# Kernel tuning notes

Measured on AMD Instinct MI355X. Metric: run time of the kernel, lower is better.

The kernel has to match this reference:

```python
import jax, jax.numpy as jnp
import numpy as np

D_MODEL = 1024
NUM_HEADS = 16
D_K = D_MODEL // NUM_HEADS
D_FF = 4096
EPS = 1e-5


def setup_inputs() -> dict:
    key = jax.random.key(0)
    ks = jax.random.split(key, 16)
    B, S = 2, 2048
    s_attn = 1.0 / np.sqrt(D_MODEL)
    s_ff1 = 1.0 / np.sqrt(D_MODEL)
    s_ff2 = 1.0 / np.sqrt(D_FF)
    return {
        "x": jax.random.normal(ks[0], (B, S, D_MODEL), jnp.float32),
        "Wq": jax.random.normal(ks[1], (D_MODEL, D_MODEL), jnp.float32) * s_attn,
        "bq": jnp.zeros((D_MODEL,), jnp.float32),
        "Wk": jax.random.normal(ks[2], (D_MODEL, D_MODEL), jnp.float32) * s_attn,
        "bk": jnp.zeros((D_MODEL,), jnp.float32),
        "Wv": jax.random.normal(ks[3], (D_MODEL, D_MODEL), jnp.float32) * s_attn,
        "bv": jnp.zeros((D_MODEL,), jnp.float32),
        "Wo": jax.random.normal(ks[4], (D_MODEL, D_MODEL), jnp.float32) * s_attn,
        "bo": jnp.zeros((D_MODEL,), jnp.float32),
        "W1": jax.random.normal(ks[5], (D_MODEL, D_FF), jnp.float32) * s_ff1,
        "b1": jnp.zeros((D_FF,), jnp.float32),
        "W2": jax.random.normal(ks[6], (D_FF, D_MODEL), jnp.float32) * s_ff2,
        "b2": jnp.zeros((D_MODEL,), jnp.float32),
        "g1": jnp.ones((D_MODEL,), jnp.float32),
        "be1": jnp.zeros((D_MODEL,), jnp.float32),
        "g2": jnp.ones((D_MODEL,), jnp.float32),
        "be2": jnp.zeros((D_MODEL,), jnp.float32),
    }


def _layernorm(x, g, b):
    m = jnp.mean(x, axis=-1, keepdims=True)
    v = jnp.mean(jnp.square(x - m), axis=-1, keepdims=True)
    return (x - m) * jax.lax.rsqrt(v + EPS) * g + b


def _split_heads(x, B, S):
    # (B, S, D) -> (B, H, S, d_k)
    return x.reshape(B, S, NUM_HEADS, D_K).transpose(0, 2, 1, 3)


def reference(x, Wq, bq, Wk, bk, Wv, bv, Wo, bo, W1, b1, W2, b2, g1, be1, g2, be2):
    B, S, _ = x.shape
    Q = _split_heads(x @ Wq + bq, B, S)
    K = _split_heads(x @ Wk + bk, B, S)
    V = _split_heads(x @ Wv + bv, B, S)
    scores = jnp.einsum("bhqd,bhkd->bhqk", Q, K) / np.sqrt(D_K).astype(np.float32)
    attn = jax.nn.softmax(scores, axis=-1)  # dropout is identity (p=0 / eval)
    ctx = jnp.einsum("bhqk,bhkd->bhqd", attn, V)
    ctx = ctx.transpose(0, 2, 1, 3).reshape(B, S, D_MODEL)
    attn_out = ctx @ Wo + bo
    h = _layernorm(x + attn_out, g1, be1)
    ff = jax.nn.relu(h @ W1 + b1) @ W2 + b2
    out = _layernorm(h + ff, g2, be2)
    return out, attn
```

## Files before the change

### kernel.cpp

```cpp
#include <hip/hip_runtime.h>
#include <cstddef>
#include <cstdint>

#define D_MODEL 1024
#define NUM_HEADS 16
#define DK 64
#define D_FF 4096
#define SEQ 2048
#define BATCH 2
#define EPS 1e-5f

typedef unsigned short u16;
typedef __attribute__((ext_vector_type(8))) short bf16x8;
typedef __attribute__((ext_vector_type(8))) unsigned short us8;
typedef __attribute__((ext_vector_type(4))) unsigned short us4;
typedef __attribute__((ext_vector_type(4))) float f32x4;

#define SBAR() asm volatile("s_barrier" ::: "memory")

__device__ __forceinline__ u16 f2b(float f) {
    unsigned u = __float_as_uint(f);
    u += 0x7fffu + ((u >> 16) & 1u);
    return (u16)(u >> 16);
}
__device__ __forceinline__ float b2f(u16 v) {
    return __uint_as_float((unsigned)v << 16);
}

__device__ __forceinline__ void gload16(const void* g, void* l) {
    __builtin_amdgcn_global_load_lds(
        (const __attribute__((address_space(1))) void*)g,
        (__attribute__((address_space(3))) void*)l, 16, 0, 0);
}

__device__ __forceinline__ void stage_half(
    const u16* __restrict__ g, int ld, long kbase, int h,
    u16* dst, int tid, int wid)
{
#pragma unroll
    for (int r = 0; r < 2; ++r) {
        const int ci  = r * 512 + tid;
        const int row = ci >> 2;
        const int wd  = ci & 3;
        const int f   = (row + (row >> 2)) & 3;
        const long src = (long)row * ld + kbase + (long)(h * 4 + (wd ^ f)) * 8;
        gload16(g + src, dst + (r * 512 + wid * 64) * 8);
    }
}

__device__ __forceinline__ bf16x8 frag64(const u16* base, int ks, int row, int g) {
    const int f = (row + (row >> 2)) & 3;
    return *(const bf16x8*)&base[ks * 8192 + row * 32 + ((g ^ f) * 8)];
}

template<int KTOT, bool RELU>
__global__ __launch_bounds__(512, 2) void gemm256(
    const u16* __restrict__ Abf, const u16* __restrict__ BT,
    const float* __restrict__ bias0, u16* __restrict__ C0,
    int ldc, int nx)
{
    constexpr int NT = KTOT / 64;
    __shared__ u16 lds[2][32768];

    const int tid = threadIdx.x;
    const int wid = tid >> 6, l = tid & 63;
    const int r16 = l & 15, g = l >> 4;
    const int wr = wid >> 2, wc = wid & 3;

    const int nwg = gridDim.x;
    const int q = nwg >> 3, rr = nwg & 7;
    const int xcd = blockIdx.x & 7, idx = blockIdx.x >> 3;
    const int wg = (xcd < rr ? xcd * (q + 1) : rr * (q + 1) + (xcd - rr) * q) + idx;
    const long bm = (long)(wg / nx) * 256;
    const long bn = (long)(wg % nx) * 256;

    const u16* Ag = Abf + bm * KTOT;
    const u16* Bg = BT + bn * KTOT;

    f32x4 acc[8][4];
#pragma unroll
    for (int i = 0; i < 8; ++i)
#pragma unroll
        for (int n = 0; n < 4; ++n)
            acc[i][n] = (f32x4){0.f, 0.f, 0.f, 0.f};

    stage_half(Ag, KTOT, 0, 0, &lds[0][0],     tid, wid);
    stage_half(Ag, KTOT, 0, 1, &lds[0][8192],  tid, wid);
    stage_half(Bg, KTOT, 0, 0, &lds[0][16384], tid, wid);
    stage_half(Bg, KTOT, 0, 1, &lds[0][24576], tid, wid);
    if (NT > 1) {
        stage_half(Ag, KTOT, 64, 0, &lds[1][0],     tid, wid);
        stage_half(Bg, KTOT, 64, 0, &lds[1][16384], tid, wid);
    }
    asm volatile("s_waitcnt vmcnt(4)" ::: "memory");
    SBAR();

    for (int t = 0; t < NT; ++t) {
        u16* cur = &lds[t & 1][0];
        u16* nxt = &lds[(t + 1) & 1][0];
        const long k1 = (long)(t + 1) * 64;
        const long k2 = (long)(t + 2) * 64;
        const bool s1 = (t + 1 < NT), s2 = (t + 2 < NT);

        bf16x8 a0[4], b0[4];
#pragma unroll
        for (int i = 0; i < 4; ++i) {
            a0[i] = frag64(cur,         0, wr * 128 + i * 16 + r16, g);
            b0[i] = frag64(cur + 16384, 0, wc * 64  + i * 16 + r16, g);
        }
        if (s1) stage_half(Ag, KTOT, k1, 1, nxt + 8192, tid, wid);
        SBAR();
        __builtin_amdgcn_s_setprio(1);
#pragma unroll
        for (int i = 0; i < 4; ++i)
#pragma unroll
            for (int n = 0; n < 4; ++n)
                acc[i][n] = __builtin_amdgcn_mfma_f32_16x16x32_bf16(
                    a0[i], b0[n], acc[i][n], 0, 0, 0);
        __builtin_amdgcn_s_setprio(0);
        SBAR();

        bf16x8 a1[4];
#pragma unroll
        for (int i = 0; i < 4; ++i)
            a1[i] = frag64(cur, 0, wr * 128 + (i + 4) * 16 + r16, g);
        if (s1) stage_half(Bg, KTOT, k1, 1, nxt + 24576, tid, wid);
        SBAR();
        __builtin_amdgcn_s_setprio(1);
#pragma unroll
        for (int i = 0; i < 4; ++i)
#pragma unroll
            for (int n = 0; n < 4; ++n)
                acc[i + 4][n] = __builtin_amdgcn_mfma_f32_16x16x32_bf16(
                    a1[i], b0[n], acc[i + 4][n], 0, 0, 0);
        __builtin_amdgcn_s_setprio(0);
        SBAR();

        bf16x8 a2[4], b1[4];
#pragma unroll
        for (int i = 0; i < 4; ++i) {
            a2[i] = frag64(cur,         1, wr * 128 + i * 16 + r16, g);
            b1[i] = frag64(cur + 16384, 1, wc * 64  + i * 16 + r16, g);
        }
        if (s2) stage_half(Ag, KTOT, k2, 0, cur, tid, wid);
        SBAR();
        __builtin_amdgcn_s_setprio(1);
#pragma unroll
        for (int i = 0; i < 4; ++i)
#pragma unroll
            for (int n = 0; n < 4; ++n)
                acc[i][n] = __builtin_amdgcn_mfma_f32_16x16x32_bf16(
                    a2[i], b1[n], acc[i][n], 0, 0, 0);
        __builtin_amdgcn_s_setprio(0);
        SBAR();

        bf16x8 a3[4];
#pragma unroll
        for (int i = 0; i < 4; ++i)
            a3[i] = frag64(cur, 1, wr * 128 + (i + 4) * 16 + r16, g);
        if (s2) stage_half(Bg, KTOT, k2, 0, cur + 16384, tid, wid);
        SBAR();
        __builtin_amdgcn_s_setprio(1);
#pragma unroll
        for (int i = 0; i < 4; ++i)
#pragma unroll
            for (int n = 0; n < 4; ++n)
                acc[i + 4][n] = __builtin_amdgcn_mfma_f32_16x16x32_bf16(
                    a3[i], b1[n], acc[i + 4][n], 0, 0, 0);
        __builtin_amdgcn_s_setprio(0);
        if (s2)      asm volatile("s_waitcnt vmcnt(4)" ::: "memory");
        else if (s1) asm volatile("s_waitcnt vmcnt(0)" ::: "memory");
        SBAR();
    }

    const long crow0 = bm + wr * 128 + g * 4;
    const long ccol0 = bn + wc * 64 + r16;
#pragma unroll
    for (int n = 0; n < 4; ++n) {
        const long col = ccol0 + n * 16;
        const float bv = bias0[col];
#pragma unroll
        for (int i = 0; i < 8; ++i)
#pragma unroll
            for (int j = 0; j < 4; ++j) {
                const long row = crow0 + i * 16 + j;
                float v = acc[i][n][j] + bv;
                if (RELU) v = fmaxf(v, 0.f);
                C0[row * (long)ldc + col] = f2b(v);
            }
    }
}

template<bool RELU, int NSPLIT>
__global__ __launch_bounds__(256) void gemm_mfma(
    const u16* __restrict__ Abf, const u16* __restrict__ BT,
    const float* __restrict__ bias0, const float* __restrict__ bias1,
    const float* __restrict__ bias2,
    u16* __restrict__ C0, u16* __restrict__ C1, u16* __restrict__ C2,
    int lda, int ldb, int ldc, int K, int nx)
{
    constexpr int BM = 128, BN = 128;
    constexpr int MI = 4, NI = 4;
    constexpr int RA = 2, RB = 2;
    constexpr int TILE = (BM + BN) * 32;

    __shared__ u16 sm[3][TILE];

    const int tid = threadIdx.x;
    const int w = tid >> 6, l = tid & 63;
    const int r16 = l & 15, g = l >> 4;
    const int wr = w >> 1, wc = w & 1;

    const int nwg = gridDim.x;
    const int q = nwg >> 3, rr = nwg & 7;
    const int xcd = blockIdx.x & 7, idx = blockIdx.x >> 3;
    const int wg = (xcd < rr ? xcd * (q + 1) : rr * (q + 1) + (xcd - rr) * q) + idx;
    const long bm = (long)(wg / nx) * BM;
    const long bn = (long)(wg % nx) * BN;

    f32x4 acc[MI][NI];
#pragma unroll
    for (int mi = 0; mi < MI; ++mi)
#pragma unroll
        for (int ni = 0; ni < NI; ++ni)
            acc[mi][ni] = (f32x4){0.f, 0.f, 0.f, 0.f};

    long aOff[RA], bOff[RB];
#pragma unroll
    for (int r = 0; r < RA; ++r) {
        int c = r * 256 + tid;
        aOff[r] = (long)(bm + (c >> 2)) * lda + (c & 3) * 8;
    }
#pragma unroll
    for (int r = 0; r < RB; ++r) {
        int c = r * 256 + tid;
        bOff[r] = (long)(bn + (c >> 2)) * ldb + (c & 3) * 8;
    }

#pragma unroll
    for (int r = 0; r < RA; ++r)
        gload16(Abf + aOff[r], &sm[0][0] + (r * 256 + w * 64) * 8);
#pragma unroll
    for (int r = 0; r < RB; ++r)
        gload16(BT + bOff[r], &sm[0][BM * 32] + (r * 256 + w * 64) * 8);
    if (K > 32) {
#pragma unroll
        for (int r = 0; r < RA; ++r)
            gload16(Abf + aOff[r] + 32, &sm[1][0] + (r * 256 + w * 64) * 8);
#pragma unroll
        for (int r = 0; r < RB; ++r)
            gload16(BT + bOff[r] + 32, &sm[1][BM * 32] + (r * 256 + w * 64) * 8);
    }
    asm volatile("s_waitcnt vmcnt(4)" ::: "memory");
    SBAR();

    int cur = 0;
    for (int k0 = 0; k0 < K; k0 += 32) {
        const int nx2 = (cur >= 1) ? cur - 1 : cur + 2;
        if (k0 + 64 < K) {
#pragma unroll
            for (int r = 0; r < RA; ++r)
                gload16(Abf + aOff[r] + k0 + 64, &sm[nx2][0] + (r * 256 + w * 64) * 8);
#pragma unroll
            for (int r = 0; r < RB; ++r)
                gload16(BT + bOff[r] + k0 + 64, &sm[nx2][BM * 32] + (r * 256 + w * 64) * 8);
        }

        const u16* smA = &sm[cur][0];
        const u16* smB = &sm[cur][BM * 32];
        bf16x8 af[MI], bfr[NI];
#pragma unroll
        for (int mi = 0; mi < MI; ++mi)
            af[mi] = *(const bf16x8*)&smA[(wr * 64 + mi * 16 + r16) * 32 + g * 8];
#pragma unroll
        for (int ni = 0; ni < NI; ++ni)
            bfr[ni] = *(const bf16x8*)&smB[(wc * 64 + ni * 16 + r16) * 32 + g * 8];
#pragma unroll
        for (int mi = 0; mi < MI; ++mi)
#pragma unroll
            for (int ni = 0; ni < NI; ++ni)
                acc[mi][ni] = __builtin_amdgcn_mfma_f32_16x16x32_bf16(
                    af[mi], bfr[ni], acc[mi][ni], 0, 0, 0);

        if (k0 + 64 < K)      asm volatile("s_waitcnt vmcnt(4)" ::: "memory");
        else if (k0 + 32 < K) asm volatile("s_waitcnt vmcnt(0)" ::: "memory");
        SBAR();
        cur = (cur == 2) ? 0 : cur + 1;
    }

    u16* Cb = C0; const float* bp = bias0; long coff = 0;
    if (NSPLIT == 3) {
        const int grp = (int)(bn >> 10);
        if (grp == 1)      { Cb = C1; bp = bias1; }
        else if (grp == 2) { Cb = C2; bp = bias2; }
        coff = (long)grp << 10;
    }
    const long crow0 = bm + wr * 64 + g * 4;
    const long ccol0 = bn + wc * 64 + r16 - coff;
#pragma unroll
    for (int ni = 0; ni < NI; ++ni) {
        const long col = ccol0 + ni * 16;
        const float bv = bp[col];
#pragma unroll
        for (int mi = 0; mi < MI; ++mi) {
#pragma unroll
            for (int j = 0; j < 4; ++j) {
                const long row = crow0 + mi * 16 + j;
                float v = acc[mi][ni][j] + bv;
                if (RELU) v = fmaxf(v, 0.f);
                Cb[row * (long)ldc + col] = f2b(v);
            }
        }
    }
}

template<bool RELU>
__global__ __launch_bounds__(256) void gemm_n64(
    const u16* __restrict__ Abf, const u16* __restrict__ BT,
    const float* __restrict__ bias, u16* __restrict__ C,
    int lda, int ldb, int ldc, int K, int nx)
{
    constexpr int TILE = 12288;
    __shared__ u16 sm[3][TILE];

    const int tid = threadIdx.x;
    const int w = tid >> 6, l = tid & 63;
    const int r16 = l & 15, g = l >> 4;

    const int nwg = gridDim.x;
    const int q = nwg >> 3, rr = nwg & 7;
    const int xcd = blockIdx.x & 7, idx = blockIdx.x >> 3;
    const int wg = (xcd < rr ? xcd * (q + 1) : rr * (q + 1) + (xcd - rr) * q) + idx;
    const long bm = (long)(wg / nx) * 128;
    const long bn = (long)(wg % nx) * 64;

    f32x4 acc[2][4];
#pragma unroll
    for (int mi = 0; mi < 2; ++mi)
#pragma unroll
        for (int ni = 0; ni < 4; ++ni)
            acc[mi][ni] = (f32x4){0.f, 0.f, 0.f, 0.f};

    long aOff[4], bOff[2];
#pragma unroll
    for (int r = 0; r < 4; ++r) {
        int c = r * 256 + tid;
        int row = c >> 3, sl = c & 7;
        aOff[r] = (long)(bm + row) * lda + (long)(sl ^ (row & 7)) * 8;
    }
#pragma unroll
    for (int r = 0; r < 2; ++r) {
        int c = r * 256 + tid;
        int row = c >> 3, sl = c & 7;
        bOff[r] = (long)(bn + row) * ldb + (long)(sl ^ (row & 7)) * 8;
    }

#define N64_STAGE(buf, koff)                                                  \
    {                                                                         \
        _Pragma("unroll")                                                     \
        for (int r = 0; r < 4; ++r)                                           \
            gload16(Abf + aOff[r] + (koff), &sm[buf][0] + (r * 256 + w * 64) * 8); \
        _Pragma("unroll")                                                     \
        for (int r = 0; r < 2; ++r)                                           \
            gload16(BT + bOff[r] + (koff), &sm[buf][8192] + (r * 256 + w * 64) * 8); \
    }

    N64_STAGE(0, 0)
    if (K > 64) N64_STAGE(1, 64)
    asm volatile("s_waitcnt vmcnt(6)" ::: "memory");
    SBAR();

    int cur = 0;
    for (int k0 = 0; k0 < K; k0 += 64) {
        const int nx2 = (cur >= 1) ? cur - 1 : cur + 2;
        if (k0 + 128 < K) N64_STAGE(nx2, k0 + 128)

        const u16* smA = &sm[cur][0];
        const u16* smB = &sm[cur][8192];
#pragma unroll
        for (int ks = 0; ks < 2; ++ks) {
            bf16x8 af[2], bfr[4];
#pragma unroll
            for (int mi = 0; mi < 2; ++mi)
                af[mi] = *(const bf16x8*)
                    &smA[(w * 32 + mi * 16 + r16) * 64 + (((ks * 4 + g) ^ (r16 & 7)) * 8)];
#pragma unroll
            for (int ni = 0; ni < 4; ++ni)
                bfr[ni] = *(const bf16x8*)
                    &smB[(ni * 16 + r16) * 64 + (((ks * 4 + g) ^ (r16 & 7)) * 8)];
            __builtin_amdgcn_s_setprio(1);
#pragma unroll
            for (int mi = 0; mi < 2; ++mi)
#pragma unroll
                for (int ni = 0; ni < 4; ++ni)
                    acc[mi][ni] = __builtin_amdgcn_mfma_f32_16x16x32_bf16(
                        af[mi], bfr[ni], acc[mi][ni], 0, 0, 0);
            __builtin_amdgcn_s_setprio(0);
        }

        if (k0 + 128 < K)      asm volatile("s_waitcnt vmcnt(6)" ::: "memory");
        else if (k0 + 64 < K)  asm volatile("s_waitcnt vmcnt(0)" ::: "memory");
        SBAR();
        cur = (cur == 2) ? 0 : cur + 1;
    }
#undef N64_STAGE

    const long crow0 = bm + w * 32 + g * 4;
    const long ccol0 = bn + r16;
#pragma unroll
    for (int ni = 0; ni < 4; ++ni) {
        const long col = ccol0 + ni * 16;
        const float bv = bias[col];
#pragma unroll
        for (int mi = 0; mi < 2; ++mi) {
#pragma unroll
            for (int j = 0; j < 4; ++j) {
                const long row = crow0 + mi * 16 + j;
                float v = acc[mi][ni][j] + bv;
                if (RELU) v = fmaxf(v, 0.f);
                C[row * (long)ldc + col] = f2b(v);
            }
        }
    }
}

#define QBLK 128
#define KB2 128
#define NT2 (SEQ / KB2)
#define C2E 0.18033688f

__global__ __launch_bounds__(256) void flash_attn(
    const u16* __restrict__ Qg, const u16* __restrict__ Kg,
    const u16* __restrict__ Vt, float* __restrict__ attn,
    u16* __restrict__ ctx)
{
    __shared__ u16 smem[32768];
    __shared__ u16 Ps[4][2048];

    const int tid = threadIdx.x;
    const int w = tid >> 6, l = tid & 63;
    const int r16 = l & 15, g = l >> 4;

    const int wg = (blockIdx.x & 7) * (gridDim.x >> 3) + (blockIdx.x >> 3);
    const int qb = wg & 15, z = wg >> 4;
    const int b = z >> 4, h = z & 15;
    const long q0 = (long)qb * QBLK;

    const long kBase = ((long)b * SEQ) * D_MODEL + h * DK;
    const long vBase = (long)z * DK * SEQ;

    u16* const Qs = smem + 24576;

#pragma unroll
    for (int r = 0; r < 4; ++r) {
        int c = r * 256 + tid;
        int row = c >> 3, bl = c & 7;
        gload16(Qg + ((long)b * SEQ + q0 + row) * D_MODEL + h * DK + ((bl ^ (row & 7)) * 8),
                Qs + (r * 256 + w * 64) * 8);
    }
#define STAGE_K(dst, kro)                                                     \
    {                                                                         \
        _Pragma("unroll")                                                     \
        for (int r = 0; r < 4; ++r) {                                         \
            int c = r * 256 + tid;                                            \
            int row = c >> 3, bl = c & 7;                                     \
            gload16(Kg + kBase + ((kro) + row) * (long)D_MODEL + ((bl ^ (row & 7)) * 8), \
                    (dst) + (r * 256 + w * 64) * 8);                          \
        }                                                                     \
    }
#define STAGE_V(dst, kro)                                                     \
    {                                                                         \
        _Pragma("unroll")                                                     \
        for (int r = 0; r < 4; ++r) {                                         \
            int c = r * 256 + tid;                                            \
            int row = c >> 4, bl = c & 15;                                    \
            gload16(Vt + vBase + (long)row * SEQ + (kro) + ((bl ^ (row & 15)) * 8), \
                    (dst) + (r * 256 + w * 64) * 8);                          \
        }                                                                     \
    }

    STAGE_K(smem, 0)
    STAGE_K(smem + 16384, KB2)
    __syncthreads();

    bf16x8 qf[2][2];
#pragma unroll
    for (int qi = 0; qi < 2; ++qi)
#pragma unroll
        for (int ks = 0; ks < 2; ++ks)
            qf[qi][ks] = *(const bf16x8*)
                &Qs[(w * 32 + qi * 16 + r16) * 64 + (((ks * 4 + g) ^ (r16 & 7)) * 8)];
    __syncthreads();

    float lrun[2] = {0.f, 0.f};

    for (int t = 0; t < NT2; ++t) {
        const int m3n = (t + 2) % 3;
        u16* kdst = (m3n == 0) ? smem : (m3n == 1) ? smem + 16384 : smem + 8192;
        if (t + 2 < NT2) STAGE_K(kdst, (long)(t + 2) * KB2)
        const int m3c = t % 3;
        const u16* kcur = (m3c == 0) ? smem : (m3c == 1) ? smem + 16384 : smem + 8192;

#pragma unroll
        for (int sub = 0; sub < 2; ++sub) {
            f32x4 sT[4][2];
#pragma unroll
            for (int ki = 0; ki < 4; ++ki)
#pragma unroll
                for (int qi = 0; qi < 2; ++qi) sT[ki][qi] = (f32x4){0.f, 0.f, 0.f, 0.f};

            __builtin_amdgcn_s_setprio(1);
#pragma unroll
            for (int ks = 0; ks < 2; ++ks) {
                bf16x8 kf[4];
#pragma unroll
                for (int ki = 0; ki < 4; ++ki)
                    kf[ki] = *(const bf16x8*)
                        &kcur[(sub * 64 + ki * 16 + r16) * 64 + (((ks * 4 + g) ^ (r16 & 7)) * 8)];
#pragma unroll
                for (int ki = 0; ki < 4; ++ki)
#pragma unroll
                    for (int qi = 0; qi < 2; ++qi)
                        sT[ki][qi] = __builtin_amdgcn_mfma_f32_16x16x32_bf16(
                            kf[ki], qf[qi][ks], sT[ki][qi], 0, 0, 0);
            }
            __builtin_amdgcn_s_setprio(0);

#pragma unroll
            for (int qi = 0; qi < 2; ++qi) {
                float ls = 0.f;
#pragma unroll
                for (int ki = 0; ki < 4; ++ki)
#pragma unroll
                    for (int j = 0; j < 4; ++j)
                        ls += exp2f(sT[ki][qi][j] * C2E);
                ls += __shfl_xor(ls, 16);
                ls += __shfl_xor(ls, 32);
                lrun[qi] += ls;
            }
        }
        if (t + 2 < NT2)      asm volatile("s_waitcnt vmcnt(4)" ::: "memory");
        else if (t + 1 < NT2) asm volatile("s_waitcnt vmcnt(0)" ::: "memory");
        if (t + 1 < NT2) SBAR();
    }

    const float il[2] = {1.0f / lrun[0], 1.0f / lrun[1]};

    __syncthreads();
    STAGE_K(smem, 0)
    STAGE_V(smem + 8192, 0)
    __syncthreads();

    f32x4 acc2[2][4];
#pragma unroll
    for (int mi = 0; mi < 2; ++mi)
#pragma unroll
        for (int ni = 0; ni < 4; ++ni) acc2[mi][ni] = (f32x4){0.f, 0.f, 0.f, 0.f};

    const long arow0 = ((long)z * SEQ + q0 + w * 32) * (long)SEQ;

    for (int t = 0; t < NT2; ++t) {
        const int k0 = t * KB2;
        if (t + 1 < NT2) {
            u16* dst = smem + ((t + 1) & 1) * 16384;
            STAGE_K(dst, (long)(t + 1) * KB2)
            STAGE_V(dst + 8192, (long)(t + 1) * KB2)
        }
        const u16* kcur = smem + (t & 1) * 16384;
        const u16* vcur = kcur + 8192;

#pragma unroll
        for (int sub = 0; sub < 2; ++sub) {
            f32x4 sT[4][2];
#pragma unroll
            for (int ki = 0; ki < 4; ++ki)
#pragma unroll
                for (int qi = 0; qi < 2; ++qi) sT[ki][qi] = (f32x4){0.f, 0.f, 0.f, 0.f};

            __builtin_amdgcn_s_setprio(1);
#pragma unroll
            for (int ks = 0; ks < 2; ++ks) {
                bf16x8 kf[4];
#pragma unroll
                for (int ki = 0; ki < 4; ++ki)
                    kf[ki] = *(const bf16x8*)
                        &kcur[(sub * 64 + ki * 16 + r16) * 64 + (((ks * 4 + g) ^ (r16 & 7)) * 8)];
#pragma unroll
                for (int ki = 0; ki < 4; ++ki)
#pragma unroll
                    for (int qi = 0; qi < 2; ++qi)
                        sT[ki][qi] = __builtin_amdgcn_mfma_f32_16x16x32_bf16(
                            kf[ki], qf[qi][ks], sT[ki][qi], 0, 0, 0);
            }
            __builtin_amdgcn_s_setprio(0);

#pragma unroll
            for (int qi = 0; qi < 2; ++qi) {
                const long ar = arow0 + (long)(qi * 16 + r16) * SEQ + k0 + sub * 64 + g * 4;
                const int prow = (qi * 16 + r16) * 64;
#pragma unroll
                for (int ki = 0; ki < 4; ++ki) {
                    f32x4 p;
                    p[0] = exp2f(sT[ki][qi][0] * C2E) * il[qi];
                    p[1] = exp2f(sT[ki][qi][1] * C2E) * il[qi];
                    p[2] = exp2f(sT[ki][qi][2] * C2E) * il[qi];
                    p[3] = exp2f(sT[ki][qi][3] * C2E) * il[qi];
                    __builtin_nontemporal_store(p, (f32x4*)&attn[ar + ki * 16]);
                    us4 pb;
                    pb[0] = f2b(p[0]); pb[1] = f2b(p[1]);
                    pb[2] = f2b(p[2]); pb[3] = f2b(p[3]);
                    const int kblk = 2 * ki + (g >> 1);
                    *(us4*)&Ps[w][prow + ((kblk ^ (r16 & 7)) << 3) + ((g & 1) << 2)] = pb;
                }
            }

            __builtin_amdgcn_s_setprio(1);
#pragma unroll
            for (int ks = 0; ks < 2; ++ks) {
                bf16x8 pf[2], vf[4];
#pragma unroll
                for (int mi = 0; mi < 2; ++mi)
                    pf[mi] = *(const bf16x8*)
                        &Ps[w][(mi * 16 + r16) * 64 + (((ks * 4 + g) ^ (r16 & 7)) << 3)];
#pragma unroll
                for (int ni = 0; ni < 4; ++ni) {
                    const int row = ni * 16 + r16;
                    const int slot = sub * 8 + ks * 4 + g;
                    vf[ni] = *(const bf16x8*)
                        &vcur[row * 128 + ((slot ^ (row & 15)) * 8)];
                }
#pragma unroll
                for (int mi = 0; mi < 2; ++mi)
#pragma unroll
                    for (int ni = 0; ni < 4; ++ni)
                        acc2[mi][ni] = __builtin_amdgcn_mfma_f32_16x16x32_bf16(
                            pf[mi], vf[ni], acc2[mi][ni], 0, 0, 0);
            }
            __builtin_amdgcn_s_setprio(0);
        }

        if (t + 1 < NT2) {
            asm volatile("s_waitcnt vmcnt(16)" ::: "memory");
            SBAR();
        }
    }
#undef STAGE_K
#undef STAGE_V

#pragma unroll
    for (int mi = 0; mi < 2; ++mi)
#pragma unroll
        for (int j = 0; j < 4; ++j) {
            const long grow = (long)b * SEQ + q0 + w * 32 + mi * 16 + g * 4 + j;
#pragma unroll
            for (int ni = 0; ni < 4; ++ni)
                ctx[grow * D_MODEL + h * DK + ni * 16 + r16] = f2b(acc2[mi][ni][j]);
        }
}

__device__ __forceinline__ void tr32(
    const float* __restrict__ W, u16* __restrict__ Wt, int R, int C,
    int bx, int by, int tx, int ty, float (*t)[33])
{
    const long c = (long)bx * 32 + tx;
    const long r0 = (long)by * 32;
#pragma unroll
    for (int j = 0; j < 32; j += 8)
        t[ty + j][tx] = W[(r0 + ty + j) * C + c];
    __syncthreads();
    const long r = r0 + tx;
#pragma unroll
    for (int j = 0; j < 32; j += 8)
        Wt[((long)bx * 32 + ty + j) * R + r] = f2b(t[tx][ty + j]);
}

__global__ __launch_bounds__(256) void preproc(
    const float* __restrict__ x, u16* __restrict__ x_bf,
    const float* __restrict__ Wq, const float* __restrict__ Wk,
    const float* __restrict__ Wv, const float* __restrict__ Wo,
    u16* __restrict__ Wqkvo_t,
    const float* __restrict__ W1, u16* __restrict__ W1t,
    const float* __restrict__ W2, u16* __restrict__ W2t)
{
    __shared__ float t[32][33];
    int bid = blockIdx.x;
    const int tx = threadIdx.x & 31, ty = threadIdx.x >> 5;

    if (bid < 2048) {
        long i = ((long)bid * 256 + threadIdx.x) * 8;
        float4 a = *(const float4*)(x + i);
        float4 b = *(const float4*)(x + i + 4);
        us8 o;
        o[0] = f2b(a.x); o[1] = f2b(a.y); o[2] = f2b(a.z); o[3] = f2b(a.w);
        o[4] = f2b(b.x); o[5] = f2b(b.y); o[6] = f2b(b.z); o[7] = f2b(b.w);
        *(us8*)(x_bf + i) = o;
        return;
    }
    bid -= 2048;
    if (bid < 4096) {
        const int z = bid >> 10, rem = bid & 1023;
        const float* W = (z == 0) ? Wq : (z == 1) ? Wk : (z == 2) ? Wv : Wo;
        tr32(W, Wqkvo_t + (size_t)z * D_MODEL * D_MODEL, D_MODEL, D_MODEL,
             rem & 31, rem >> 5, tx, ty, t);
        return;
    }
    bid -= 4096;
    if (bid < 4096) {
        tr32(W1, W1t, D_MODEL, D_FF, bid & 127, bid >> 7, tx, ty, t);
        return;
    }
    bid -= 4096;
    {
        tr32(W2, W2t, D_FF, D_MODEL, bid & 31, bid >> 5, tx, ty, t);
    }
}

__global__ __launch_bounds__(256) void transpose_v(
    const u16* __restrict__ V, u16* __restrict__ Vt)
{
    __shared__ u16 t[32][33];
    const int z = blockIdx.z, b = z >> 4, h = z & 15;
    const int tx = threadIdx.x & 31, ty = threadIdx.x >> 5;
    const long k0 = (long)blockIdx.x * 32;
    const long d0 = (long)blockIdx.y * 32;
#pragma unroll
    for (int j = 0; j < 32; j += 8)
        t[ty + j][tx] = V[((long)b * SEQ + k0 + ty + j) * D_MODEL + h * DK + d0 + tx];
    __syncthreads();
#pragma unroll
    for (int j = 0; j < 32; j += 8)
        Vt[((long)z * DK + d0 + ty + j) * SEQ + k0 + tx] = t[tx][ty + j];
}

template<int OM>
__global__ __launch_bounds__(256) void add_ln_kernel(
    const u16* __restrict__ a, const u16* __restrict__ b,
    const float* __restrict__ g, const float* __restrict__ be,
    void* __restrict__ outp)
{
    const int l = threadIdx.x & 63, w = threadIdx.x >> 6;
    const long row = (long)blockIdx.x * 4 + w;
    const long base = row * D_MODEL;

    float xv[16];
#pragma unroll
    for (int c = 0; c < 2; ++c) {
        const long off = c * 512 + l * 8;
        us8 av = *(const us8*)(a + base + off);
        us8 bv = *(const us8*)(b + base + off);
#pragma unroll
        for (int i = 0; i < 8; ++i)
            xv[c * 8 + i] = b2f(av[i]) + b2f(bv[i]);
    }

    float s = 0.f;
#pragma unroll
    for (int i = 0; i < 16; ++i) s += xv[i];
#pragma unroll
    for (int off = 1; off < 64; off <<= 1) s += __shfl_xor(s, off);
    const float mean = s * (1.0f / D_MODEL);

    float ss = 0.f;
#pragma unroll
    for (int i = 0; i < 16; ++i) {
        xv[i] -= mean;
        ss += xv[i] * xv[i];
    }
#pragma unroll
    for (int off = 1; off < 64; off <<= 1) ss += __shfl_xor(ss, off);
    const float rs = rsqrtf(ss * (1.0f / D_MODEL) + EPS);

#pragma unroll
    for (int c = 0; c < 2; ++c) {
        const long off = c * 512 + l * 8;
        float4 g0 = *(const float4*)(g + off);
        float4 g1 = *(const float4*)(g + off + 4);
        float4 b0 = *(const float4*)(be + off);
        float4 b1 = *(const float4*)(be + off + 4);
        float o[8];
        o[0] = xv[c*8+0] * rs * g0.x + b0.x;
        o[1] = xv[c*8+1] * rs * g0.y + b0.y;
        o[2] = xv[c*8+2] * rs * g0.z + b0.z;
        o[3] = xv[c*8+3] * rs * g0.w + b0.w;
        o[4] = xv[c*8+4] * rs * g1.x + b1.x;
        o[5] = xv[c*8+5] * rs * g1.y + b1.y;
        o[6] = xv[c*8+6] * rs * g1.z + b1.z;
        o[7] = xv[c*8+7] * rs * g1.w + b1.w;
        if (OM == 0) {
            float4 v0 = {o[0], o[1], o[2], o[3]};
            float4 v1 = {o[4], o[5], o[6], o[7]};
            *(float4*)((float*)outp + base + off) = v0;
            *(float4*)((float*)outp + base + off + 4) = v1;
        } else {
            us8 ob;
#pragma unroll
            for (int i = 0; i < 8; ++i) ob[i] = f2b(o[i]);
            *(us8*)((u16*)outp + base + off) = ob;
        }
    }
}

extern "C" void kernel_launch(void* const* d_in, const int* in_sizes, int n_in,
                              void* d_out, int out_size, void* d_ws, size_t ws_size,
                              hipStream_t stream)
{
    const float* x   = (const float*)d_in[0];
    const float* Wq  = (const float*)d_in[1];
    const float* bq  = (const float*)d_in[2];
    const float* Wk  = (const float*)d_in[3];
    const float* bk  = (const float*)d_in[4];
    const float* Wv  = (const float*)d_in[5];
    const float* bv  = (const float*)d_in[6];
    const float* Wo  = (const float*)d_in[7];
    const float* bo  = (const float*)d_in[8];
    const float* W1  = (const float*)d_in[9];
    const float* b1  = (const float*)d_in[10];
    const float* W2  = (const float*)d_in[11];
    const float* b2  = (const float*)d_in[12];
    const float* g1  = (const float*)d_in[13];
    const float* be1 = (const float*)d_in[14];
    const float* g2  = (const float*)d_in[15];
    const float* be2 = (const float*)d_in[16];

    float* out  = (float*)d_out;
    float* attn = out + (size_t)BATCH * SEQ * D_MODEL;

    char* ws = (char*)d_ws;
    const size_t MB = 1u << 20;
    u16* x_bf    = (u16*)(ws);
    u16* Q_bf    = (u16*)(ws + 8 * MB);
    u16* K_bf    = (u16*)(ws + 16 * MB);
    u16* Vt      = (u16*)(ws + 24 * MB);
    u16* V_bf    = (u16*)(ws + 32 * MB);
    u16* Wqkvo_t = (u16*)(ws + 40 * MB);
    u16* W1t     = (u16*)(ws + 48 * MB);
    u16* W2t     = (u16*)(ws + 56 * MB);
    u16* ff1_bf  = (u16*)(ws + 64 * MB);
    u16* ctx_bf  = (u16*)(ws + 96 * MB);
    u16* Wot     = Wqkvo_t + (size_t)3 * D_MODEL * D_MODEL;
    u16* h_bf    = K_bf;
    u16* ao_bf   = V_bf;
    u16* ff2_bf  = Vt;

    const int M = BATCH * SEQ;
    dim3 T(256);

    preproc<<<dim3(2048 + 3 * 4096), T, 0, stream>>>(
        x, x_bf, Wq, Wk, Wv, Wo, Wqkvo_t, W1, W1t, W2, W2t);

    gemm_mfma<false, 3><<<dim3((M / 128) * 24), T, 0, stream>>>(
        x_bf, Wqkvo_t, bq, bk, bv, Q_bf, K_bf, V_bf,
        D_MODEL, D_MODEL, D_MODEL, D_MODEL, 24);

    transpose_v<<<dim3(SEQ / 32, DK / 32, BATCH * NUM_HEADS), T, 0, stream>>>(V_bf, Vt);

    flash_attn<<<dim3((SEQ / QBLK) * BATCH * NUM_HEADS), T, 0, stream>>>(
        Q_bf, K_bf, Vt, attn, ctx_bf);

    gemm_n64<false><<<dim3((M / 128) * 16), T, 0, stream>>>(
        ctx_bf, Wot, bo, ao_bf, D_MODEL, D_MODEL, D_MODEL, D_MODEL, 16);

    add_ln_kernel<1><<<dim3(M / 4), T, 0, stream>>>(x_bf, ao_bf, g1, be1, h_bf);

    gemm256<D_MODEL, true><<<dim3((M / 256) * (D_FF / 256)), dim3(512), 0, stream>>>(
        h_bf, W1t, b1, ff1_bf, D_FF, D_FF / 256);

    gemm_n64<false><<<dim3((M / 128) * 16), T, 0, stream>>>(
        ff1_bf, W2t, b2, ff2_bf, D_FF, D_FF, D_MODEL, D_FF, 16);

    add_ln_kernel<0><<<dim3(M / 4), T, 0, stream>>>(h_bf, ff2_bf, g2, be2, out);
}
```

Baseline: 384.6 us.

## Fuse V transpose into QKV GEMM epilogue and prefetch flash pass-two tiles

The QKV GEMM now writes the V third of its output already transposed into the head-major Vt layout, staging through swizzled LDS, so the separate transpose_v kernel and its round trip through global memory are removed. The flash attention kernel issues the first K/V tile loads for the second pass during the last iteration of the first pass and flips its double-buffer parity, replacing two block-wide syncs with a waitcnt and barrier. The preprocessing kernel uses nontemporal loads for the fp32 inputs. The risks are LDS reuse hazards in the epilogue and buffer-aliasing mistakes in the new prefetch schedule.

Result: no change. 386.6 us (+0.5%).

```diff
diff --git a/kernel.cpp b/kernel.cpp
--- a/kernel.cpp
+++ b/kernel.cpp
@@ -288,11 +288,45 @@
         cur = (cur == 2) ? 0 : cur + 1;
     }
 
+    if (NSPLIT == 3 && bn >= 2048) {
+        u16* ldsT = (u16*)&sm[0][0];
+        __syncthreads();
+        const int cb = wc * 64 + r16;
+        const int rb = wr * 64 + g * 4;
+#pragma unroll
+        for (int ni = 0; ni < NI; ++ni) {
+            const int c = cb + ni * 16;
+            const float bv = bias2[(int)(bn - 2048) + c];
+            const int sw = (c & 7) << 3;
+#pragma unroll
+            for (int mi = 0; mi < MI; ++mi) {
+                const int r0 = rb + mi * 16;
+                us4 pv;
+#pragma unroll
+                for (int j = 0; j < 4; ++j) pv[j] = f2b(acc[mi][ni][j] + bv);
+                *(us4*)&ldsT[c * 128 + (r0 ^ sw)] = pv;
+            }
+        }
+        __syncthreads();
+        const int btok = (int)(bm >> 11);
+        const long kb = bm & 2047;
+        const int chunk = tid & 15;
+#pragma unroll
+        for (int pass = 0; pass < 8; ++pass) {
+            const int c = pass * 16 + (tid >> 4);
+            const int vcol = (int)(bn - 2048) + c;
+            const int h = vcol >> 6, d = vcol & 63;
+            const long vrow = ((long)(btok * 16 + h) * 64 + d) * (long)SEQ;
+            us8 v = *(const us8*)&ldsT[c * 128 + ((chunk * 8) ^ ((c & 7) << 3))];
+            *(us8*)&C2[vrow + kb + chunk * 8] = v;
+        }
+        return;
+    }
+
     u16* Cb = C0; const float* bp = bias0; long coff = 0;
     if (NSPLIT == 3) {
         const int grp = (int)(bn >> 10);
-        if (grp == 1)      { Cb = C1; bp = bias1; }
-        else if (grp == 2) { Cb = C2; bp = bias2; }
+        if (grp == 1) { Cb = C1; bp = bias1; }
         coff = (long)grp << 10;
     }
     const long crow0 = bm + wr * 64 + g * 4;
@@ -498,6 +532,10 @@
         const int m3n = (t + 2) % 3;
         u16* kdst = (m3n == 0) ? smem : (m3n == 1) ? smem + 16384 : smem + 8192;
         if (t + 2 < NT2) STAGE_K(kdst, (long)(t + 2) * KB2)
+        if (t == NT2 - 1) {
+            STAGE_K(smem + 16384, 0)
+            STAGE_V(smem + 24576, 0)
+        }
         const int m3c = t % 3;
         const u16* kcur = (m3c == 0) ? smem : (m3c == 1) ? smem + 16384 : smem + 8192;
 
@@ -546,10 +584,8 @@
 
     const float il[2] = {1.0f / lrun[0], 1.0f / lrun[1]};
 
-    __syncthreads();
-    STAGE_K(smem, 0)
-    STAGE_V(smem + 8192, 0)
-    __syncthreads();
+    asm volatile("s_waitcnt vmcnt(0)" ::: "memory");
+    SBAR();
 
     f32x4 acc2[2][4];
 #pragma unroll
@@ -562,11 +598,11 @@
     for (int t = 0; t < NT2; ++t) {
         const int k0 = t * KB2;
         if (t + 1 < NT2) {
-            u16* dst = smem + ((t + 1) & 1) * 16384;
+            u16* dst = smem + (t & 1) * 16384;
             STAGE_K(dst, (long)(t + 1) * KB2)
             STAGE_V(dst + 8192, (long)(t + 1) * KB2)
         }
-        const u16* kcur = smem + (t & 1) * 16384;
+        const u16* kcur = smem + (((t + 1) & 1)) * 16384;
         const u16* vcur = kcur + 8192;
 
 #pragma unroll
@@ -666,7 +702,7 @@
     const long r0 = (long)by * 32;
 #pragma unroll
     for (int j = 0; j < 32; j += 8)
-        t[ty + j][tx] = W[(r0 + ty + j) * C + c];
+        t[ty + j][tx] = __builtin_nontemporal_load(&W[(r0 + ty + j) * C + c]);
     __syncthreads();
     const long r = r0 + tx;
 #pragma unroll
@@ -688,11 +724,11 @@
 
     if (bid < 2048) {
         long i = ((long)bid * 256 + threadIdx.x) * 8;
-        float4 a = *(const float4*)(x + i);
-        float4 b = *(const float4*)(x + i + 4);
+        f32x4 a = __builtin_nontemporal_load((const f32x4*)(x + i));
+        f32x4 b = __builtin_nontemporal_load((const f32x4*)(x + i + 4));
         us8 o;
-        o[0] = f2b(a.x); o[1] = f2b(a.y); o[2] = f2b(a.z); o[3] = f2b(a.w);
-        o[4] = f2b(b.x); o[5] = f2b(b.y); o[6] = f2b(b.z); o[7] = f2b(b.w);
+        o[0] = f2b(a[0]); o[1] = f2b(a[1]); o[2] = f2b(a[2]); o[3] = f2b(a[3]);
+        o[4] = f2b(b[0]); o[5] = f2b(b[1]); o[6] = f2b(b[2]); o[7] = f2b(b[3]);
         *(us8*)(x_bf + i) = o;
         return;
     }
@@ -713,23 +749,6 @@
     {
         tr32(W2, W2t, D_FF, D_MODEL, bid & 31, bid >> 5, tx, ty, t);
     }
-}
-
-__global__ __launch_bounds__(256) void transpose_v(
-    const u16* __restrict__ V, u16* __restrict__ Vt)
-{
-    __shared__ u16 t[32][33];
-    const int z = blockIdx.z, b = z >> 4, h = z & 15;
-    const int tx = threadIdx.x & 31, ty = threadIdx.x >> 5;
-    const long k0 = (long)blockIdx.x * 32;
-    const long d0 = (long)blockIdx.y * 32;
-#pragma unroll
-    for (int j = 0; j < 32; j += 8)
-        t[ty + j][tx] = V[((long)b * SEQ + k0 + ty + j) * D_MODEL + h * DK + d0 + tx];
-    __syncthreads();
-#pragma unroll
-    for (int j = 0; j < 32; j += 8)
-        Vt[((long)z * DK + d0 + ty + j) * SEQ + k0 + tx] = t[tx][ty + j];
 }
 
 template<int OM>
@@ -831,7 +850,7 @@
     u16* Q_bf    = (u16*)(ws + 8 * MB);
     u16* K_bf    = (u16*)(ws + 16 * MB);
     u16* Vt      = (u16*)(ws + 24 * MB);
-    u16* V_bf    = (u16*)(ws + 32 * MB);
+    u16* ao_bf   = (u16*)(ws + 32 * MB);
     u16* Wqkvo_t = (u16*)(ws + 40 * MB);
     u16* W1t     = (u16*)(ws + 48 * MB);
     u16* W2t     = (u16*)(ws + 56 * MB);
@@ -839,7 +858,6 @@
     u16* ctx_bf  = (u16*)(ws + 96 * MB);
     u16* Wot     = Wqkvo_t + (size_t)3 * D_MODEL * D_MODEL;
     u16* h_bf    = K_bf;
-    u16* ao_bf   = V_bf;
     u16* ff2_bf  = Vt;
 
     const int M = BATCH * SEQ;
@@ -849,10 +867,8 @@
         x, x_bf, Wq, Wk, Wv, Wo, Wqkvo_t, W1, W1t, W2, W2t);
 
     gemm_mfma<false, 3><<<dim3((M / 128) * 24), T, 0, stream>>>(
-        x_bf, Wqkvo_t, bq, bk, bv, Q_bf, K_bf, V_bf,
+        x_bf, Wqkvo_t, bq, bk, bv, Q_bf, K_bf, Vt,
         D_MODEL, D_MODEL, D_MODEL, D_MODEL, 24);
-
-    transpose_v<<<dim3(SEQ / 32, DK / 32, BATCH * NUM_HEADS), T, 0, stream>>>(V_bf, Vt);
 
     flash_attn<<<dim3((SEQ / QBLK) * BATCH * NUM_HEADS), T, 0, stream>>>(
         Q_bf, K_bf, Vt, attn, ctx_bf);
```
